# Performance work log

Hardware: AMD Instinct MI355X
Metric: run time of the kernel (lower is better)

The kernel has to match this reference:

```python
import jax, jax.numpy as jnp
import numpy as np

GENRES = 20; TAGS = 1000; GTAGS = 1128; MOVIES = 20000; YEARS = 120; TBINS = 128
B = 1024; HIST = 50; PH = 256; OD = 128
EG = 8; ET = 16; EGT = 16; EM = 32; EY = 8; EUG = 32; ETS = 4
PAD = MOVIES  # padding index; context buffers have MOVIES+1 rows, last row = zeros


def setup_inputs():
    ks = iter(jax.random.split(jax.random.key(0), 64))
    nrm = lambda shp, s=0.1: (s * jax.random.normal(next(ks), shp)).astype(jnp.float32)
    P = MOVIES + 1
    genome_ctx = jax.random.uniform(next(ks), (P, GTAGS), dtype=jnp.float32).at[-1].set(0.0)
    genre_ctx = jax.random.uniform(next(ks), (P, GENRES), dtype=jnp.float32).at[-1].set(0.0)
    tag_ctx = jax.random.uniform(next(ks), (P, TAGS), dtype=jnp.float32).at[-1].set(0.0)
    year_ctx = jax.random.randint(next(ks), (P,), 0, YEARS).at[-1].set(0)
    return dict(
        user_genre_contexts=jax.random.uniform(next(ks), (B, GENRES), dtype=jnp.float32),
        user_watch_history=jax.random.randint(next(ks), (B, HIST), 0, P),
        user_watch_history_ratings=5.0 * jax.random.uniform(next(ks), (B, HIST), dtype=jnp.float32),
        timestamps=jax.random.randint(next(ks), (B,), 0, TBINS),
        target_movieId=jax.random.randint(next(ks), (B,), 0, MOVIES),
        genome_ctx=genome_ctx, genre_ctx=genre_ctx, tag_ctx=tag_ctx, year_ctx=year_ctx,
        item_emb=nrm((P, EM), 0.01).at[-1].set(0.0),  # padding_idx row zeroed
        year_emb_tab=nrm((YEARS, EY), 0.01),
        ts_emb_tab=nrm((TBINS, ETS), 0.01),
        w_item=nrm((EM, EM)), b_item=jnp.zeros((EM,), jnp.float32),
        w_genre=nrm((GENRES, EG)), b_genre=jnp.zeros((EG,), jnp.float32),
        w_tag=nrm((TAGS, ET)), b_tag=jnp.zeros((ET,), jnp.float32),
        w_genome=nrm((GTAGS, EGT)), b_genome=jnp.zeros((EGT,), jnp.float32),
        w_year=nrm((EY, EY)), b_year=jnp.zeros((EY,), jnp.float32),
        w_ugenre=nrm((GENRES, EUG)), b_ugenre=jnp.zeros((EUG,), jnp.float32),
        w_ts=nrm((ETS, ETS)), b_ts=jnp.zeros((ETS,), jnp.float32),
        w_up1=nrm((OD + EGT + EUG + ETS, PH)), b_up1=jnp.zeros((PH,), jnp.float32),
        w_up2=nrm((PH, OD)), b_up2=jnp.zeros((OD,), jnp.float32),
        w_ip1=nrm((EG + ET + EGT + EM + EY, PH)), b_ip1=jnp.zeros((PH,), jnp.float32),
        w_ip2=nrm((PH, OD)), b_ip2=jnp.zeros((OD,), jnp.float32),
    )


def reference(user_genre_contexts, user_watch_history, user_watch_history_ratings,
              timestamps, target_movieId, genome_ctx, genre_ctx, tag_ctx, year_ctx,
              item_emb, year_emb_tab, ts_emb_tab,
              w_item, b_item, w_genre, b_genre, w_tag, b_tag, w_genome, b_genome,
              w_year, b_year, w_ugenre, b_ugenre, w_ts, b_ts,
              w_up1, b_up1, w_up2, b_up2, w_ip1, b_ip1, w_ip2, b_ip2):
    lt = lambda x, W, b: jnp.tanh(x @ W + b)

    def item_tower(mg, mt, mgt, yr, ids):
        # concat of five small Linear+Tanh towers, then 2-layer projection MLP
        cat = jnp.concatenate([
            lt(mg, w_genre, b_genre), lt(mt, w_tag, b_tag), lt(mgt, w_genome, b_genome),
            lt(item_emb[ids], w_item, b_item), lt(year_emb_tab[yr], w_year, b_year)], axis=-1)
        return jax.nn.relu(cat @ w_ip1 + b_ip1) @ w_ip2 + b_ip2

    Bn, Hn = user_watch_history.shape
    pad_mask = (user_watch_history != PAD).astype(jnp.float32)[..., None]       # (B,H,1)
    rating_weights = user_watch_history_ratings[..., None] * pad_mask            # (B,H,1)
    weight_sum = jnp.clip(jnp.abs(rating_weights).sum(axis=1), 1e-6)             # (B,1)

    # item pool: full item-tower embeddings of watched movies, rating-weighted avg
    flat = user_watch_history.reshape(-1)
    embs = item_tower(genre_ctx[flat], tag_ctx[flat], genome_ctx[flat],
                      year_ctx[flat], flat).reshape(Bn, Hn, OD)
    item_pool = (embs * rating_weights).sum(axis=1) / weight_sum                 # (B,OD)

    # genome pool (kept separately in use_item_pool_for_history mode)
    genome_embs = lt(genome_ctx[user_watch_history], w_genome, b_genome)         # (B,H,EGT)
    genome_emb = (genome_embs * rating_weights).sum(axis=1) / weight_sum

    genre_emb = lt(user_genre_contexts, w_ugenre, b_ugenre)
    ts_emb = lt(ts_emb_tab[timestamps], w_ts, b_ts)
    user_cat = jnp.concatenate([item_pool, genome_emb, genre_emb, ts_emb], axis=1)
    user = jax.nn.relu(user_cat @ w_up1 + b_up1) @ w_up2 + b_up2                 # (B,OD)

    item = item_tower(genre_ctx[target_movieId], tag_ctx[target_movieId],
                      genome_ctx[target_movieId], year_ctx[target_movieId], target_movieId)
    return jnp.einsum('bd,bd->b', user, item)
```

## Files before the change

kernel.cpp:

```cpp
#include <hip/hip_runtime.h>
#include <hip/hip_bf16.h>

typedef __bf16 bf16x8 __attribute__((ext_vector_type(8)));
typedef __bf16 bf16x4 __attribute__((ext_vector_type(4)));
typedef float  f32x4  __attribute__((ext_vector_type(4)));

namespace {
constexpr int P       = 20001;
constexpr int NT_TILE = 1251;
constexpr int PROWS   = NT_TILE * 16;
constexpr int NGENRES = 20;
constexpr int NTAGS   = 1000;
constexpr int NGTAGS  = 1128;
constexpr int NB      = 1024;
constexpr int NH      = 50;
constexpr int PHID    = 256;
constexpr int OD      = 128;
constexpr int EG = 8, ET = 16, EGT = 16, EM = 32, EY = 8, EUG = 32, ETS = 4;
constexpr int PAD  = 20000;
constexpr int SAW  = 1160;
constexpr int SC   = 104;
constexpr int SH   = 264;
constexpr int UC   = 192;
constexpr int UCS  = 200;
constexpr int KC_TAG = 32, KC_GEN = 36;
constexpr int KC_IP1 = 3,  NT_IP1 = 16;
constexpr int KC_IP2 = 8,  NT_IP2 = 8;
constexpr int KC_UP1 = 6,  NT_UP1 = 16;
constexpr int KC_UP2 = 8,  NT_UP2 = 8;
}

static __device__ __forceinline__ f32x4 mfma16(bf16x8 a, bf16x8 b, f32x4 c) {
  return __builtin_amdgcn_mfma_f32_16x16x32_bf16(a, b, c, 0, 0, 0);
}

__global__ __launch_bounds__(512) void setup_wf_kernel(
    const float* __restrict__ w_tag, const float* __restrict__ w_genome,
    const float* __restrict__ w_ip1, const float* __restrict__ w_ip2,
    const float* __restrict__ w_up1, const float* __restrict__ w_up2,
    __bf16* __restrict__ Wtf, __bf16* __restrict__ Wgf,
    __bf16* __restrict__ Wip1f, __bf16* __restrict__ Wip2f,
    __bf16* __restrict__ Wup1f, __bf16* __restrict__ Wup2f)
{
  const int b = blockIdx.x, t = threadIdx.x;
  const int l = t >> 3, j = t & 7;
  const int krow = (l >> 4) * 8 + j, l15 = l & 15;
  const float* src; __bf16* dst; int K, N, kc, nt;
  if (b < 32)        { src = w_tag;    dst = Wtf   + (long)b * 512;       K = NTAGS;  N = 16;  kc = b;      nt = 0; }
  else if (b < 68)   { int i = b - 32;  src = w_genome; dst = Wgf   + (long)i * 512; K = NGTAGS; N = 16;  kc = i;      nt = 0; }
  else if (b < 116)  { int i = b - 68;  src = w_ip1;    dst = Wip1f + (long)i * 512; K = 80;     N = 256; kc = i / 16; nt = i % 16; }
  else if (b < 180)  { int i = b - 116; src = w_ip2;    dst = Wip2f + (long)i * 512; K = 256;    N = 128; kc = i / 8;  nt = i % 8; }
  else if (b < 276)  { int i = b - 180; src = w_up1;    dst = Wup1f + (long)i * 512; K = 180;    N = 256; kc = i / 16; nt = i % 16; }
  else               { int i = b - 276; src = w_up2;    dst = Wup2f + (long)i * 512; K = 256;    N = 128; kc = i / 8;  nt = i % 8; }
  const int k = kc * 32 + krow, n = nt * 16 + l15;
  float v = (k < K) ? src[(long)k * N + n] : 0.f;
  dst[t] = (__bf16)v;
}

__global__ __launch_bounds__(256) void tower_kernel(
    const float* __restrict__ tag_ctx, const float* __restrict__ genome_ctx,
    const float* __restrict__ genre_ctx, const int* __restrict__ year_ctx,
    const float* __restrict__ item_emb, const float* __restrict__ year_tab,
    const float* __restrict__ w_genre, const float* __restrict__ b_genre,
    const float* __restrict__ b_tag,   const float* __restrict__ b_genome,
    const float* __restrict__ w_item,  const float* __restrict__ b_item,
    const float* __restrict__ w_year,  const float* __restrict__ b_year,
    const float* __restrict__ b_ip1,   const float* __restrict__ b_ip2,
    const __bf16* __restrict__ Wtf,   const __bf16* __restrict__ Wgf,
    const __bf16* __restrict__ Wip1f, const __bf16* __restrict__ Wip2f,
    float* __restrict__ T, float* __restrict__ GT)
{
  union ShU { __bf16 a[16][SAW]; __bf16 h[16][SH]; };
  __shared__ __align__(16) ShU u;
  __shared__ __align__(16) __bf16 s_cat[16][SC];
  __shared__ __align__(16) f32x4  s_red[3][64];

  const int t = threadIdx.x, tile = blockIdx.x;
  const int wave = t >> 6, lane = t & 63, l15 = lane & 15, quad = lane >> 4;
  const int r = t >> 4, c16 = t & 15;
  const long rid = min(tile * 16 + r, P - 1);

  {
    const float* row = tag_ctx + rid * NTAGS;
    #pragma unroll
    for (int i = 0; i < 16; ++i) {
      int f = c16 + i * 16;
      if (f < 250) {
        float4 v = *(const float4*)(row + f * 4);
        bf16x4 b4 = {(__bf16)v.x, (__bf16)v.y, (__bf16)v.z, (__bf16)v.w};
        *(bf16x4*)&u.a[r][f * 4] = b4;
      }
    }
    if (c16 < 8) *(bf16x4*)&u.a[r][NTAGS + c16 * 4] = (bf16x4){(__bf16)0.f,(__bf16)0.f,(__bf16)0.f,(__bf16)0.f};
  }
  __syncthreads();

  f32x4 accT = {0.f, 0.f, 0.f, 0.f};
  #pragma unroll
  for (int kc = 0; kc < 8; ++kc) {
    const int kcg = wave * 8 + kc;
    bf16x8 a  = *(const bf16x8*)&u.a[l15][kcg * 32 + quad * 8];
    bf16x8 bb = *(const bf16x8*)(Wtf + ((long)kcg * 64 + lane) * 8);
    accT = mfma16(a, bb, accT);
  }
  if (wave > 0) s_red[wave - 1][lane] = accT;
  __syncthreads();

  {
    const float* row = genome_ctx + rid * NGTAGS;
    #pragma unroll
    for (int i = 0; i < 18; ++i) {
      int f = c16 + i * 16;
      if (f < 282) {
        float4 v = *(const float4*)(row + f * 4);
        bf16x4 b4 = {(__bf16)v.x, (__bf16)v.y, (__bf16)v.z, (__bf16)v.w};
        *(bf16x4*)&u.a[r][f * 4] = b4;
      }
    }
    if (c16 < 8) *(bf16x4*)&u.a[r][NGTAGS + c16 * 4] = (bf16x4){(__bf16)0.f,(__bf16)0.f,(__bf16)0.f,(__bf16)0.f};
  }
  if (wave == 0) {
    accT += s_red[0][lane]; accT += s_red[1][lane]; accT += s_red[2][lane];
    const float bt = b_tag[l15];
    #pragma unroll
    for (int r2 = 0; r2 < 4; ++r2)
      s_cat[quad * 4 + r2][EG + l15] = (__bf16)tanhf(accT[r2] + bt);
  }
  __syncthreads();

  f32x4 accG = {0.f, 0.f, 0.f, 0.f};
  #pragma unroll
  for (int kc = 0; kc < 9; ++kc) {
    const int kcg = wave * 9 + kc;
    bf16x8 a  = *(const bf16x8*)&u.a[l15][kcg * 32 + quad * 8];
    bf16x8 bb = *(const bf16x8*)(Wgf + ((long)kcg * 64 + lane) * 8);
    accG = mfma16(a, bb, accG);
  }
  if (wave > 0) s_red[wave - 1][lane] = accG;
  __syncthreads();

  if (wave == 0) {
    accG += s_red[0][lane]; accG += s_red[1][lane]; accG += s_red[2][lane];
    const float bg = b_genome[l15];
    #pragma unroll
    for (int r2 = 0; r2 < 4; ++r2) {
      int m = quad * 4 + r2;
      float v = tanhf(accG[r2] + bg);
      s_cat[m][EG + ET + l15] = (__bf16)v;
      GT[(long)(tile * 16 + m) * EGT + l15] = v;
    }
  }
  {
    const int m = r, j = c16;
    const long id = rid;
    if (j < 8) {
      const float* rg = genre_ctx + id * NGENRES;
      float a = b_genre[j];
      #pragma unroll
      for (int k = 0; k < NGENRES; ++k) a = fmaf(rg[k], w_genre[k * EG + j], a);
      s_cat[m][j] = (__bf16)tanhf(a);
      s_cat[m][80 + j] = (__bf16)0.f;
      s_cat[m][88 + j] = (__bf16)0.f;
    } else {
      const int jj = j - 8;
      const int yr = year_ctx[id];
      float a = b_year[jj];
      #pragma unroll
      for (int k = 0; k < EY; ++k)
        a = fmaf(year_tab[yr * EY + k], w_year[k * EY + jj], a);
      s_cat[m][72 + jj] = (__bf16)tanhf(a);
    }
    const float* e = item_emb + id * EM;
    float a0 = b_item[2 * j], a1 = b_item[2 * j + 1];
    #pragma unroll 8
    for (int k = 0; k < EM; ++k) {
      float ev = e[k];
      a0 = fmaf(ev, w_item[k * EM + 2 * j], a0);
      a1 = fmaf(ev, w_item[k * EM + 2 * j + 1], a1);
    }
    s_cat[m][40 + 2 * j]     = (__bf16)tanhf(a0);
    s_cat[m][40 + 2 * j + 1] = (__bf16)tanhf(a1);
  }
  __syncthreads();

  {
    bf16x8 af[KC_IP1];
    #pragma unroll
    for (int kc = 0; kc < KC_IP1; ++kc)
      af[kc] = *(const bf16x8*)&s_cat[l15][kc * 32 + quad * 8];
    #pragma unroll
    for (int nt = 0; nt < 4; ++nt) {
      const int n = wave * 64 + nt * 16 + l15;
      const float bb = b_ip1[n];
      f32x4 acc = {bb, bb, bb, bb};
      #pragma unroll
      for (int kc = 0; kc < KC_IP1; ++kc) {
        bf16x8 bfr = *(const bf16x8*)(Wip1f + ((long)(kc * NT_IP1 + wave * 4 + nt) * 64 + lane) * 8);
        acc = mfma16(af[kc], bfr, acc);
      }
      #pragma unroll
      for (int r2 = 0; r2 < 4; ++r2)
        u.h[quad * 4 + r2][n] = (__bf16)fmaxf(acc[r2], 0.f);
    }
  }
  __syncthreads();

  {
    bf16x8 af[KC_IP2];
    #pragma unroll
    for (int kc = 0; kc < KC_IP2; ++kc)
      af[kc] = *(const bf16x8*)&u.h[l15][kc * 32 + quad * 8];
    #pragma unroll
    for (int nt = 0; nt < 2; ++nt) {
      const int n = wave * 32 + nt * 16 + l15;
      const float bb = b_ip2[n];
      f32x4 acc = {bb, bb, bb, bb};
      #pragma unroll
      for (int kc = 0; kc < KC_IP2; ++kc) {
        bf16x8 bfr = *(const bf16x8*)(Wip2f + ((long)(kc * NT_IP2 + wave * 2 + nt) * 64 + lane) * 8);
        acc = mfma16(af[kc], bfr, acc);
      }
      #pragma unroll
      for (int r2 = 0; r2 < 4; ++r2)
        T[(long)(tile * 16 + quad * 4 + r2) * OD + n] = acc[r2];
    }
  }
}

__global__ __launch_bounds__(256) void user_pool_kernel(
    const float* __restrict__ ugc, const int* __restrict__ hist,
    const float* __restrict__ ratings, const int* __restrict__ tstamps,
    const float* __restrict__ ts_tab,
    const float* __restrict__ w_ugenre, const float* __restrict__ b_ugenre,
    const float* __restrict__ w_ts, const float* __restrict__ b_ts,
    const float* __restrict__ T, const float* __restrict__ GT,
    __bf16* __restrict__ Ucat)
{
  __shared__ float s_w[64];
  __shared__ int   s_ids[64];
  __shared__ float s_part[2][OD];
  __shared__ float s_gp[8][EGT];
  __shared__ float s_inv;

  const int b = blockIdx.x, t = threadIdx.x;

  if (t < 64) {
    int id = PAD; float w = 0.f;
    if (t < NH) {
      id = hist[b * NH + t];
      float r = ratings[b * NH + t];
      w = (id != PAD) ? r : 0.f;
    }
    s_ids[t] = id; s_w[t] = w;
    float s = fabsf(w);
    #pragma unroll
    for (int off = 32; off; off >>= 1) s += __shfl_xor(s, off, 64);
    if (t == 0) s_inv = 1.f / fmaxf(s, 1e-6f);
  }
  __syncthreads();
  const float inv = s_inv;

  {
    const int c = t & (OD - 1), part = t >> 7;
    float acc = 0.f;
    #pragma unroll
    for (int i = 0; i < 25; ++i) {
      const int h = part * 25 + i;
      acc = fmaf(s_w[h], T[(long)s_ids[h] * OD + c], acc);
    }
    s_part[part][c] = acc;
  }
  __syncthreads();
  if (t < OD) {
    Ucat[(long)b * UC + t] = (__bf16)((s_part[0][t] + s_part[1][t]) * inv);
  } else {
    const int uu = t - 128, col = uu & 15, part = uu >> 4;
    float acc = 0.f;
    #pragma unroll
    for (int i = 0; i < 7; ++i) {
      const int h = part * 7 + i;
      if (h < NH) acc = fmaf(s_w[h], GT[(long)s_ids[h] * EGT + col], acc);
    }
    s_gp[part][col] = acc;
  }
  __syncthreads();
  if (t < EGT) {
    float acc = 0.f;
    #pragma unroll
    for (int p = 0; p < 8; ++p) acc += s_gp[p][t];
    Ucat[(long)b * UC + OD + t] = (__bf16)(acc * inv);
  } else if (t >= 32 && t < 64) {
    const int j = t - 32;
    float a = b_ugenre[j];
    #pragma unroll
    for (int k = 0; k < NGENRES; ++k)
      a = fmaf(ugc[b * NGENRES + k], w_ugenre[k * EUG + j], a);
    Ucat[(long)b * UC + 144 + j] = (__bf16)tanhf(a);
  } else if (t >= 64 && t < 64 + ETS) {
    const int j = t - 64;
    const int ts = tstamps[b];
    float a = b_ts[j];
    #pragma unroll
    for (int k = 0; k < ETS; ++k)
      a = fmaf(ts_tab[ts * ETS + k], w_ts[k * ETS + j], a);
    Ucat[(long)b * UC + 176 + j] = (__bf16)tanhf(a);
  } else if (t >= 68 && t < 80) {
    Ucat[(long)b * UC + 180 + (t - 68)] = (__bf16)0.f;
  }
}

__global__ __launch_bounds__(256) void user_mlp_kernel(
    const int* __restrict__ target,
    const float* __restrict__ b_up1, const float* __restrict__ b_up2,
    const __bf16* __restrict__ Wup1f, const __bf16* __restrict__ Wup2f,
    const __bf16* __restrict__ Ucat, const float* __restrict__ T,
    float* __restrict__ out)
{
  __shared__ __align__(16) __bf16 s_u[16][UCS];
  __shared__ __align__(16) __bf16 s_h[16][SH];
  __shared__ __align__(16) float  s_e[16][132];
  __shared__ float s_red[2];

  const int t = threadIdx.x, blk = blockIdx.x;
  const int wave = t >> 6, lane = t & 63, l15 = lane & 15, quad = lane >> 4;
  const int u0 = blk * 16;

  {
    const int uu = t >> 4, s = t & 15;
    const __bf16* src = Ucat + (long)(u0 + uu) * UC;
    *(bf16x8*)&s_u[uu][s * 8] = *(const bf16x8*)(src + s * 8);
    if (s < 8)
      *(bf16x8*)&s_u[uu][(s + 16) * 8] = *(const bf16x8*)(src + (s + 16) * 8);
  }
  __syncthreads();

  {
    bf16x8 af[KC_UP1];
    #pragma unroll
    for (int kc = 0; kc < KC_UP1; ++kc)
      af[kc] = *(const bf16x8*)&s_u[l15][kc * 32 + quad * 8];
    #pragma unroll
    for (int nt = 0; nt < 4; ++nt) {
      const int n = wave * 64 + nt * 16 + l15;
      const float bb = b_up1[n];
      f32x4 acc = {bb, bb, bb, bb};
      #pragma unroll
      for (int kc = 0; kc < KC_UP1; ++kc) {
        bf16x8 bfr = *(const bf16x8*)(Wup1f + ((long)(kc * NT_UP1 + wave * 4 + nt) * 64 + lane) * 8);
        acc = mfma16(af[kc], bfr, acc);
      }
      #pragma unroll
      for (int r2 = 0; r2 < 4; ++r2)
        s_h[quad * 4 + r2][n] = (__bf16)fmaxf(acc[r2], 0.f);
    }
  }
  __syncthreads();

  {
    bf16x8 af[KC_UP2];
    #pragma unroll
    for (int kc = 0; kc < KC_UP2; ++kc)
      af[kc] = *(const bf16x8*)&s_h[l15][kc * 32 + quad * 8];
    #pragma unroll
    for (int nt = 0; nt < 2; ++nt) {
      const int n = wave * 32 + nt * 16 + l15;
      const float bb = b_up2[n];
      f32x4 acc = {bb, bb, bb, bb};
      #pragma unroll
      for (int kc = 0; kc < KC_UP2; ++kc) {
        bf16x8 bfr = *(const bf16x8*)(Wup2f + ((long)(kc * NT_UP2 + wave * 2 + nt) * 64 + lane) * 8);
        acc = mfma16(af[kc], bfr, acc);
      }
      #pragma unroll
      for (int r2 = 0; r2 < 4; ++r2)
        s_e[quad * 4 + r2][n] = acc[r2];
    }
  }
  __syncthreads();

  if (t < 128) {
    const int uu = t >> 3, q = t & 7;
    const int tgt = target[u0 + uu];
    const float* trow = T + (long)tgt * OD + q * 16;
    float s = 0.f;
    #pragma unroll
    for (int i = 0; i < 4; ++i) {
      float4 v = *(const float4*)(trow + i * 4);
      f32x4 e = *(const f32x4*)&s_e[uu][q * 16 + i * 4];
      s += v.x * e[0] + v.y * e[1] + v.z * e[2] + v.w * e[3];
    }
    s += __shfl_down(s, 1, 64);
    s += __shfl_down(s, 2, 64);
    s += __shfl_down(s, 4, 64);
    if (q == 0) out[u0 + uu] = s;
  }
  (void)s_red;
}

extern "C" void kernel_launch(void* const* d_in, const int* in_sizes, int n_in,
                              void* d_out, int out_size, void* d_ws, size_t ws_size,
                              hipStream_t stream) {
  const float* ugc      = (const float*)d_in[0];
  const int*   hist     = (const int*)  d_in[1];
  const float* ratings  = (const float*)d_in[2];
  const int*   tstamps  = (const int*)  d_in[3];
  const int*   target   = (const int*)  d_in[4];
  const float* genome   = (const float*)d_in[5];
  const float* genrec   = (const float*)d_in[6];
  const float* tagc     = (const float*)d_in[7];
  const int*   yearc    = (const int*)  d_in[8];
  const float* item_emb = (const float*)d_in[9];
  const float* year_tab = (const float*)d_in[10];
  const float* ts_tab   = (const float*)d_in[11];
  const float* w_item   = (const float*)d_in[12];
  const float* b_item   = (const float*)d_in[13];
  const float* w_genre  = (const float*)d_in[14];
  const float* b_genre  = (const float*)d_in[15];
  const float* w_tag    = (const float*)d_in[16];
  const float* b_tag    = (const float*)d_in[17];
  const float* w_genome = (const float*)d_in[18];
  const float* b_genome = (const float*)d_in[19];
  const float* w_year   = (const float*)d_in[20];
  const float* b_year   = (const float*)d_in[21];
  const float* w_ugenre = (const float*)d_in[22];
  const float* b_ugenre = (const float*)d_in[23];
  const float* w_ts     = (const float*)d_in[24];
  const float* b_ts     = (const float*)d_in[25];
  const float* w_up1    = (const float*)d_in[26];
  const float* b_up1    = (const float*)d_in[27];
  const float* w_up2    = (const float*)d_in[28];
  const float* b_up2    = (const float*)d_in[29];
  const float* w_ip1    = (const float*)d_in[30];
  const float* b_ip1    = (const float*)d_in[31];
  const float* w_ip2    = (const float*)d_in[32];
  const float* b_ip2    = (const float*)d_in[33];

  char* ws = (char*)d_ws;
  size_t off = 0;
  float*  T     = (float*) (ws + off); off += (size_t)PROWS * OD * 4;
  float*  GT    = (float*) (ws + off); off += (size_t)PROWS * EGT * 4;
  __bf16* Ucat  = (__bf16*)(ws + off); off += (size_t)NB * UC * 2;
  __bf16* Wtf   = (__bf16*)(ws + off); off += (size_t)KC_TAG * 512 * 2;
  __bf16* Wgf   = (__bf16*)(ws + off); off += (size_t)KC_GEN * 512 * 2;
  __bf16* Wip1f = (__bf16*)(ws + off); off += (size_t)KC_IP1 * NT_IP1 * 512 * 2;
  __bf16* Wip2f = (__bf16*)(ws + off); off += (size_t)KC_IP2 * NT_IP2 * 512 * 2;
  __bf16* Wup1f = (__bf16*)(ws + off); off += (size_t)KC_UP1 * NT_UP1 * 512 * 2;
  __bf16* Wup2f = (__bf16*)(ws + off); off += (size_t)KC_UP2 * NT_UP2 * 512 * 2;

  setup_wf_kernel<<<dim3(340), dim3(512), 0, stream>>>(
      w_tag, w_genome, w_ip1, w_ip2, w_up1, w_up2,
      Wtf, Wgf, Wip1f, Wip2f, Wup1f, Wup2f);

  tower_kernel<<<dim3(NT_TILE), dim3(256), 0, stream>>>(
      tagc, genome, genrec, yearc, item_emb, year_tab,
      w_genre, b_genre, b_tag, b_genome, w_item, b_item, w_year, b_year,
      b_ip1, b_ip2, Wtf, Wgf, Wip1f, Wip2f, T, GT);

  user_pool_kernel<<<dim3(NB), dim3(256), 0, stream>>>(
      ugc, hist, ratings, tstamps, ts_tab,
      w_ugenre, b_ugenre, w_ts, b_ts, T, GT, Ucat);

  user_mlp_kernel<<<dim3(NB / 16), dim3(256), 0, stream>>>(
      target, b_up1, b_up2, Wup1f, Wup2f, Ucat, T, (float*)d_out);
}
```

Measured before the change: 286.1 us.

## Load tag and genome tiles together and store bf16 tower outputs for pooling

The tower kernel now stages both the tag and genome context rows into a wider shared buffer in a single phase. The two MFMA reductions then run back to back with one barrier, and separate waves finalize the tag and genome results, which removes two syncs and lets the global loads overlap. It also writes bf16 copies of the item-tower output and the genome embedding so the history pooling kernel gathers half the bytes. The cost is doubled shared memory per block, which may lower occupancy, plus an extra bf16 store of T and reduced precision in the pooled sums.

```diff
diff --git a/kernel.cpp b/kernel.cpp
--- a/kernel.cpp
+++ b/kernel.cpp
@@ -18,7 +18,8 @@
 constexpr int OD      = 128;
 constexpr int EG = 8, ET = 16, EGT = 16, EM = 32, EY = 8, EUG = 32, ETS = 4;
 constexpr int PAD  = 20000;
-constexpr int SAW  = 1160;
+constexpr int SAW  = 2184;
+constexpr int GOFF = 1024;
 constexpr int SC   = 104;
 constexpr int SH   = 264;
 constexpr int UC   = 192;
@@ -68,12 +69,13 @@
     const float* __restrict__ b_ip1,   const float* __restrict__ b_ip2,
     const __bf16* __restrict__ Wtf,   const __bf16* __restrict__ Wgf,
     const __bf16* __restrict__ Wip1f, const __bf16* __restrict__ Wip2f,
-    float* __restrict__ T, float* __restrict__ GT)
+    float* __restrict__ T, __bf16* __restrict__ Tb, __bf16* __restrict__ GTb)
 {
   union ShU { __bf16 a[16][SAW]; __bf16 h[16][SH]; };
   __shared__ __align__(16) ShU u;
   __shared__ __align__(16) __bf16 s_cat[16][SC];
-  __shared__ __align__(16) f32x4  s_red[3][64];
+  __shared__ __align__(16) f32x4  s_redT[3][64];
+  __shared__ __align__(16) f32x4  s_redG[3][64];
 
   const int t = threadIdx.x, tile = blockIdx.x;
   const int wave = t >> 6, lane = t & 63, l15 = lane & 15, quad = lane >> 4;
@@ -81,17 +83,31 @@
   const long rid = min(tile * 16 + r, P - 1);
 
   {
-    const float* row = tag_ctx + rid * NTAGS;
+    const float* rowT = tag_ctx + rid * NTAGS;
     #pragma unroll
     for (int i = 0; i < 16; ++i) {
       int f = c16 + i * 16;
       if (f < 250) {
-        float4 v = *(const float4*)(row + f * 4);
-        bf16x4 b4 = {(__bf16)v.x, (__bf16)v.y, (__bf16)v.z, (__bf16)v.w};
-        *(bf16x4*)&u.a[r][f * 4] = b4;
-      }
-    }
-    if (c16 < 8) *(bf16x4*)&u.a[r][NTAGS + c16 * 4] = (bf16x4){(__bf16)0.f,(__bf16)0.f,(__bf16)0.f,(__bf16)0.f};
+        float4 v = *(const float4*)(rowT + f * 4);
+        *(bf16x4*)&u.a[r][f * 4] =
+            (bf16x4){(__bf16)v.x, (__bf16)v.y, (__bf16)v.z, (__bf16)v.w};
+      }
+    }
+    const float* rowG = genome_ctx + rid * NGTAGS;
+    #pragma unroll
+    for (int i = 0; i < 18; ++i) {
+      int f = c16 + i * 16;
+      if (f < 282) {
+        float4 v = *(const float4*)(rowG + f * 4);
+        *(bf16x4*)&u.a[r][GOFF + f * 4] =
+            (bf16x4){(__bf16)v.x, (__bf16)v.y, (__bf16)v.z, (__bf16)v.w};
+      }
+    }
+    if (c16 < 6) {
+      const bf16x4 z = {(__bf16)0.f, (__bf16)0.f, (__bf16)0.f, (__bf16)0.f};
+      *(bf16x4*)&u.a[r][NTAGS + c16 * 4] = z;
+      *(bf16x4*)&u.a[r][GOFF + NGTAGS + c16 * 4] = z;
+    }
   }
   __syncthreads();
 
@@ -103,51 +119,33 @@
     bf16x8 bb = *(const bf16x8*)(Wtf + ((long)kcg * 64 + lane) * 8);
     accT = mfma16(a, bb, accT);
   }
-  if (wave > 0) s_red[wave - 1][lane] = accT;
-  __syncthreads();
-
-  {
-    const float* row = genome_ctx + rid * NGTAGS;
-    #pragma unroll
-    for (int i = 0; i < 18; ++i) {
-      int f = c16 + i * 16;
-      if (f < 282) {
-        float4 v = *(const float4*)(row + f * 4);
-        bf16x4 b4 = {(__bf16)v.x, (__bf16)v.y, (__bf16)v.z, (__bf16)v.w};
-        *(bf16x4*)&u.a[r][f * 4] = b4;
-      }
-    }
-    if (c16 < 8) *(bf16x4*)&u.a[r][NGTAGS + c16 * 4] = (bf16x4){(__bf16)0.f,(__bf16)0.f,(__bf16)0.f,(__bf16)0.f};
-  }
-  if (wave == 0) {
-    accT += s_red[0][lane]; accT += s_red[1][lane]; accT += s_red[2][lane];
-    const float bt = b_tag[l15];
-    #pragma unroll
-    for (int r2 = 0; r2 < 4; ++r2)
-      s_cat[quad * 4 + r2][EG + l15] = (__bf16)tanhf(accT[r2] + bt);
-  }
-  __syncthreads();
-
   f32x4 accG = {0.f, 0.f, 0.f, 0.f};
   #pragma unroll
   for (int kc = 0; kc < 9; ++kc) {
     const int kcg = wave * 9 + kc;
-    bf16x8 a  = *(const bf16x8*)&u.a[l15][kcg * 32 + quad * 8];
+    bf16x8 a  = *(const bf16x8*)&u.a[l15][GOFF + kcg * 32 + quad * 8];
     bf16x8 bb = *(const bf16x8*)(Wgf + ((long)kcg * 64 + lane) * 8);
     accG = mfma16(a, bb, accG);
   }
-  if (wave > 0) s_red[wave - 1][lane] = accG;
+  if (wave != 0) s_redT[wave - 1][lane] = accT;
+  if (wave != 1) s_redG[wave == 0 ? 0 : wave - 1][lane] = accG;
   __syncthreads();
 
   if (wave == 0) {
-    accG += s_red[0][lane]; accG += s_red[1][lane]; accG += s_red[2][lane];
+    accT += s_redT[0][lane]; accT += s_redT[1][lane]; accT += s_redT[2][lane];
+    const float bt = b_tag[l15];
+    #pragma unroll
+    for (int r2 = 0; r2 < 4; ++r2)
+      s_cat[quad * 4 + r2][EG + l15] = (__bf16)tanhf(accT[r2] + bt);
+  } else if (wave == 1) {
+    accG += s_redG[0][lane]; accG += s_redG[1][lane]; accG += s_redG[2][lane];
     const float bg = b_genome[l15];
     #pragma unroll
     for (int r2 = 0; r2 < 4; ++r2) {
       int m = quad * 4 + r2;
       float v = tanhf(accG[r2] + bg);
       s_cat[m][EG + ET + l15] = (__bf16)v;
-      GT[(long)(tile * 16 + m) * EGT + l15] = v;
+      GTb[(long)(tile * 16 + m) * EGT + l15] = (__bf16)v;
     }
   }
   {
@@ -221,8 +219,11 @@
         acc = mfma16(af[kc], bfr, acc);
       }
       #pragma unroll
-      for (int r2 = 0; r2 < 4; ++r2)
-        T[(long)(tile * 16 + quad * 4 + r2) * OD + n] = acc[r2];
+      for (int r2 = 0; r2 < 4; ++r2) {
+        const long row = tile * 16 + quad * 4 + r2;
+        T [row * OD + n] = acc[r2];
+        Tb[row * OD + n] = (__bf16)acc[r2];
+      }
     }
   }
 }
@@ -233,7 +234,7 @@
     const float* __restrict__ ts_tab,
     const float* __restrict__ w_ugenre, const float* __restrict__ b_ugenre,
     const float* __restrict__ w_ts, const float* __restrict__ b_ts,
-    const float* __restrict__ T, const float* __restrict__ GT,
+    const __bf16* __restrict__ Tb, const __bf16* __restrict__ GTb,
     __bf16* __restrict__ Ucat)
 {
   __shared__ float s_w[64];
@@ -266,7 +267,7 @@
     #pragma unroll
     for (int i = 0; i < 25; ++i) {
       const int h = part * 25 + i;
-      acc = fmaf(s_w[h], T[(long)s_ids[h] * OD + c], acc);
+      acc = fmaf(s_w[h], (float)Tb[(long)s_ids[h] * OD + c], acc);
     }
     s_part[part][c] = acc;
   }
@@ -279,7 +280,7 @@
     #pragma unroll
     for (int i = 0; i < 7; ++i) {
       const int h = part * 7 + i;
-      if (h < NH) acc = fmaf(s_w[h], GT[(long)s_ids[h] * EGT + col], acc);
+      if (h < NH) acc = fmaf(s_w[h], (float)GTb[(long)s_ids[h] * EGT + col], acc);
     }
     s_gp[part][col] = acc;
   }
@@ -319,7 +320,6 @@
   __shared__ __align__(16) __bf16 s_u[16][UCS];
   __shared__ __align__(16) __bf16 s_h[16][SH];
   __shared__ __align__(16) float  s_e[16][132];
-  __shared__ float s_red[2];
 
   const int t = threadIdx.x, blk = blockIdx.x;
   const int wave = t >> 6, lane = t & 63, l15 = lane & 15, quad = lane >> 4;
@@ -394,7 +394,6 @@
     s += __shfl_down(s, 4, 64);
     if (q == 0) out[u0 + uu] = s;
   }
-  (void)s_red;
 }
 
 extern "C" void kernel_launch(void* const* d_in, const int* in_sizes, int n_in,
@@ -438,7 +437,8 @@
   char* ws = (char*)d_ws;
   size_t off = 0;
   float*  T     = (float*) (ws + off); off += (size_t)PROWS * OD * 4;
-  float*  GT    = (float*) (ws + off); off += (size_t)PROWS * EGT * 4;
+  __bf16* Tb    = (__bf16*)(ws + off); off += (size_t)PROWS * OD * 2;
+  __bf16* GTb   = (__bf16*)(ws + off); off += (size_t)PROWS * EGT * 2;
   __bf16* Ucat  = (__bf16*)(ws + off); off += (size_t)NB * UC * 2;
   __bf16* Wtf   = (__bf16*)(ws + off); off += (size_t)KC_TAG * 512 * 2;
   __bf16* Wgf   = (__bf16*)(ws + off); off += (size_t)KC_GEN * 512 * 2;
@@ -454,11 +454,11 @@
   tower_kernel<<<dim3(NT_TILE), dim3(256), 0, stream>>>(
       tagc, genome, genrec, yearc, item_emb, year_tab,
       w_genre, b_genre, b_tag, b_genome, w_item, b_item, w_year, b_year,
-      b_ip1, b_ip2, Wtf, Wgf, Wip1f, Wip2f, T, GT);
+      b_ip1, b_ip2, Wtf, Wgf, Wip1f, Wip2f, T, Tb, GTb);
 
   user_pool_kernel<<<dim3(NB), dim3(256), 0, stream>>>(
       ugc, hist, ratings, tstamps, ts_tab,
-      w_ugenre, b_ugenre, w_ts, b_ts, T, GT, Ucat);
+      w_ugenre, b_ugenre, w_ts, b_ts, Tb, GTb, Ucat);
 
   user_mlp_kernel<<<dim3(NB / 16), dim3(256), 0, stream>>>(
       target, b_up1, b_up2, Wup1f, Wup2f, Ucat, T, (float*)d_out);
```

New measurement: 291.2 us. About the same (+1.8%).
